# Kernel optimization log

Hardware: AMD Instinct MI355X
Metric: run time of the kernel (lower is better)

Reference implementation:

```python
import jax, jax.numpy as jnp
import numpy as np
from jax import lax

B, C, H, W = 32, 256, 96, 96
G = 2            # num_groups
K = 3            # kernel_size
R = 4            # reduction_ratio
CR = C // R
BN_EPS = 1e-5


def setup_inputs() -> dict:
    key = jax.random.key(0)
    ks = jax.random.split(key, 10)
    inp = {
        "x": jax.random.normal(ks[0], (B, C, H, W), dtype=jnp.float32),
        # dynamic depthwise weight bank and bias bank
        "dyn_weight": jax.random.normal(ks[1], (G, C, K, K), dtype=jnp.float32) * 0.02,
        "dyn_bias": jax.random.normal(ks[2], (G, C), dtype=jnp.float32) * 0.02,
        # proj: ConvModule(C -> C//R, 1x1, BN, GELU)  [conv has no bias since BN follows]
        "w1": jax.random.normal(ks[3], (CR, C), dtype=jnp.float32) * (1.0 / np.sqrt(C)),
        "bn_gamma": jnp.ones((CR,), dtype=jnp.float32),
        "bn_beta": jnp.zeros((CR,), dtype=jnp.float32),
        "bn_mean": jax.random.normal(ks[4], (CR,), dtype=jnp.float32) * 0.1,
        "bn_var": jax.random.uniform(ks[5], (CR,), dtype=jnp.float32, minval=0.5, maxval=1.5),
        # second 1x1 conv: C//R -> C*G, with bias
        "w2": jax.random.normal(ks[6], (C * G, CR), dtype=jnp.float32) * (1.0 / np.sqrt(CR)),
        "b2": jnp.zeros((C * G,), dtype=jnp.float32),
    }
    return inp


def _proj(p, w1, bn_gamma, bn_beta, bn_mean, bn_var, w2, b2):
    # p: [B, C, h, w] -> [B, C*G, h, w]; 1x1 conv -> BN(eval) -> GELU -> 1x1 conv
    h = jnp.einsum('bchw,oc->bohw', p, w1)
    inv = bn_gamma * lax.rsqrt(bn_var + BN_EPS)
    h = h * inv[None, :, None, None] + (bn_beta - bn_mean * inv)[None, :, None, None]
    h = jax.nn.gelu(h, approximate=False)
    return jnp.einsum('bohw,no->bnhw', h, w2) + b2[None, :, None, None]


def reference(x, dyn_weight, dyn_bias, w1, bn_gamma, bn_beta, bn_mean, bn_var, w2, b2):
    # AdaptiveAvgPool2d to (K, K); H, W divisible by K -> uniform block average
    pooled = x.reshape(B, C, K, H // K, K, W // K).mean(axis=(3, 5))  # [B,C,K,K]

    # per-sample depthwise weights via softmax mixture over G weight banks
    scale = _proj(pooled, w1, bn_gamma, bn_beta, bn_mean, bn_var, w2, b2)
    scale = jax.nn.softmax(scale.reshape(B, G, C, K, K), axis=1)
    weight = jnp.sum(scale * dyn_weight[None], axis=1)  # [B,C,K,K]

    # per-sample bias via global-average-pooled features
    gap = x.mean(axis=(2, 3), keepdims=True)  # [B,C,1,1]
    bscale = _proj(gap, w1, bn_gamma, bn_beta, bn_mean, bn_var, w2, b2)
    bscale = jax.nn.softmax(bscale.reshape(B, G, C), axis=1)
    bias = jnp.sum(bscale * dyn_bias[None], axis=1)  # [B,C]

    # grouped conv with groups = B*C (per-sample depthwise)
    xr = x.reshape(1, B * C, H, W)
    wr = weight.reshape(B * C, 1, K, K)
    y = lax.conv_general_dilated(
        xr, wr, window_strides=(1, 1),
        padding=[(K // 2, K // 2), (K // 2, K // 2)],
        feature_group_count=B * C,
        dimension_numbers=('NCHW', 'OIHW', 'NCHW'))
    return y.reshape(B, C, H, W) + bias[:, :, None, None]
```

## Files before the change

### kernel.cpp

```cpp
#include <hip/hip_runtime.h>
#include <math.h>

#define B_ 32
#define C_ 256
#define HW_ 96
#define G_ 2
#define K_ 3
#define CR_ 64
#define IMG_ (HW_*HW_)
#define BN_EPS 1e-5f

__global__ __launch_bounds__(256) void pool_kernel(const float* __restrict__ x,
                                                   float* __restrict__ pooled) {
    int wg = blockIdx.x;
    int bh = wg % 3;
    int bc = wg / 3;
    const float4* src = (const float4*)(x + (size_t)bc * IMG_ + (size_t)bh * 32 * HW_);
    int t = threadIdx.x;
    float a0 = 0.f, a1 = 0.f, a2 = 0.f;
    #pragma unroll
    for (int k = 0; k < 3; ++k) {
        int f = t + 256 * k;
        float4 v = src[f];
        float s = v.x + v.y + v.z + v.w;
        int colq = f % 24;
        int bin = colq >> 3;
        a0 += (bin == 0) ? s : 0.f;
        a1 += (bin == 1) ? s : 0.f;
        a2 += (bin == 2) ? s : 0.f;
    }
    #pragma unroll
    for (int off = 32; off > 0; off >>= 1) {
        a0 += __shfl_down(a0, off);
        a1 += __shfl_down(a1, off);
        a2 += __shfl_down(a2, off);
    }
    __shared__ float red[3][4];
    int wave = t >> 6, lane = t & 63;
    if (lane == 0) { red[0][wave] = a0; red[1][wave] = a1; red[2][wave] = a2; }
    __syncthreads();
    if (t < 3) {
        float s = red[t][0] + red[t][1] + red[t][2] + red[t][3];
        pooled[(size_t)bc * 9 + bh * 3 + t] = s * (1.0f / 1024.0f);
    }
}

__global__ __launch_bounds__(256) void proj_kernel(
    const float* __restrict__ pooled,
    const float* __restrict__ dyn_w,
    const float* __restrict__ dyn_b,
    const float* __restrict__ w1,
    const float* __restrict__ bn_g, const float* __restrict__ bn_b,
    const float* __restrict__ bn_m, const float* __restrict__ bn_v,
    const float* __restrict__ w2,
    const float* __restrict__ b2,
    float* __restrict__ wout,
    float* __restrict__ bout)
{
    int b = blockIdx.x;
    __shared__ float pool[C_][10];
    __shared__ float hbuf[CR_][10];
    int t = threadIdx.x;

    {
        const float* p = pooled + ((size_t)b * C_ + t) * 9;
        float s = 0.f;
        #pragma unroll
        for (int i = 0; i < 9; ++i) { float v = p[i]; pool[t][i] = v; s += v; }
        pool[t][9] = s * (1.0f / 9.0f);
    }
    __syncthreads();

    for (int task = t; task < CR_ * 10; task += 256) {
        int o = task & 63, pos = task >> 6;
        const float4* wr = (const float4*)(w1 + (size_t)o * C_);
        float acc = 0.f;
        #pragma unroll 8
        for (int i = 0; i < C_ / 4; ++i) {
            float4 wv = wr[i];
            acc += wv.x * pool[4*i][pos] + wv.y * pool[4*i+1][pos]
                 + wv.z * pool[4*i+2][pos] + wv.w * pool[4*i+3][pos];
        }
        float inv = bn_g[o] * rsqrtf(bn_v[o] + BN_EPS);
        float hv = acc * inv + (bn_b[o] - bn_m[o] * inv);
        hv = 0.5f * hv * (1.0f + erff(hv * 0.70710678118654752f));
        hbuf[o][pos] = hv;
    }
    __syncthreads();

    for (int task = t; task < C_ * 10; task += 256) {
        int c = task & 255, pos = task >> 8;
        const float4* r0 = (const float4*)(w2 + (size_t)c * CR_);
        const float4* r1 = (const float4*)(w2 + (size_t)(C_ + c) * CR_);
        float s0 = b2[c], s1 = b2[C_ + c];
        #pragma unroll 8
        for (int i = 0; i < CR_ / 4; ++i) {
            float4 v0 = r0[i], v1 = r1[i];
            float h0 = hbuf[4*i][pos], h1 = hbuf[4*i+1][pos];
            float h2 = hbuf[4*i+2][pos], h3 = hbuf[4*i+3][pos];
            s0 += v0.x*h0 + v0.y*h1 + v0.z*h2 + v0.w*h3;
            s1 += v1.x*h0 + v1.y*h1 + v1.z*h2 + v1.w*h3;
        }
        float m = fmaxf(s0, s1);
        float e0 = expf(s0 - m), e1 = expf(s1 - m);
        float p0 = e0 / (e0 + e1), p1 = 1.0f - p0;
        if (pos < 9) {
            wout[((size_t)b * C_ + c) * 9 + pos] =
                p0 * dyn_w[(size_t)c * 9 + pos] + p1 * dyn_w[(size_t)(C_ * 9) + c * 9 + pos];
        } else {
            bout[(size_t)b * C_ + c] = p0 * dyn_b[c] + p1 * dyn_b[C_ + c];
        }
    }
}

__global__ __launch_bounds__(192) void dwconv_kernel(const float* __restrict__ x,
                                                     const float* __restrict__ wgt,
                                                     const float* __restrict__ bias,
                                                     float* __restrict__ out) {
    int bc = blockIdx.x;
    int t = threadIdx.x;
    int qc = t % 24;
    int rg = t / 24;
    int r0 = rg * 12;

    const float* img = x + (size_t)bc * IMG_;
    float4* dst = (float4*)(out + (size_t)bc * IMG_);

    float w[9];
    #pragma unroll
    for (int i = 0; i < 9; ++i) w[i] = wgt[(size_t)bc * 9 + i];
    float bs = bias[bc];

    float A[6], Bv[6], Cv[6];

    #define LOADROW(r, d)                                                    \
        do {                                                                 \
            int _r = (r);                                                    \
            if ((unsigned)_r < (unsigned)HW_) {                              \
                const float* _p = img + _r * HW_ + 4 * qc;                   \
                float4 _v = *(const float4*)_p;                              \
                d[1] = _v.x; d[2] = _v.y; d[3] = _v.z; d[4] = _v.w;          \
                d[0] = (qc > 0)  ? _p[-1] : 0.f;                             \
                d[5] = (qc < 23) ? _p[4]  : 0.f;                             \
            } else {                                                         \
                d[0] = d[1] = d[2] = d[3] = d[4] = d[5] = 0.f;               \
            }                                                                \
        } while (0)

    LOADROW(r0 - 1, A);
    LOADROW(r0,     Bv);

    #pragma unroll
    for (int i = 0; i < 12; ++i) {
        int r = r0 + i;
        LOADROW(r + 1, Cv);
        float4 o;
        o.x = bs; o.y = bs; o.z = bs; o.w = bs;
        #pragma unroll
        for (int j = 0; j < 3; ++j) {
            o.x += A[j]  * w[j] + Bv[j]  * w[3+j] + Cv[j]  * w[6+j];
            o.y += A[j+1]* w[j] + Bv[j+1]* w[3+j] + Cv[j+1]* w[6+j];
            o.z += A[j+2]* w[j] + Bv[j+2]* w[3+j] + Cv[j+2]* w[6+j];
            o.w += A[j+3]* w[j] + Bv[j+3]* w[3+j] + Cv[j+3]* w[6+j];
        }
        dst[r * 24 + qc] = o;
        #pragma unroll
        for (int j = 0; j < 6; ++j) { A[j] = Bv[j]; Bv[j] = Cv[j]; }
    }
    #undef LOADROW
}

extern "C" void kernel_launch(void* const* d_in, const int* in_sizes, int n_in,
                              void* d_out, int out_size, void* d_ws, size_t ws_size,
                              hipStream_t stream) {
    const float* x     = (const float*)d_in[0];
    const float* dyn_w = (const float*)d_in[1];
    const float* dyn_b = (const float*)d_in[2];
    const float* w1    = (const float*)d_in[3];
    const float* bn_g  = (const float*)d_in[4];
    const float* bn_b  = (const float*)d_in[5];
    const float* bn_m  = (const float*)d_in[6];
    const float* bn_v  = (const float*)d_in[7];
    const float* w2    = (const float*)d_in[8];
    const float* b2    = (const float*)d_in[9];
    float* out = (float*)d_out;

    float* ws = (float*)d_ws;
    float* pooled = ws;
    float* weight = ws + (size_t)B_ * C_ * 9;
    float* bias   = weight + (size_t)B_ * C_ * 9;

    pool_kernel<<<B_ * C_ * 3, 256, 0, stream>>>(x, pooled);
    proj_kernel<<<B_, 256, 0, stream>>>(pooled, dyn_w, dyn_b, w1, bn_g, bn_b,
                                        bn_m, bn_v, w2, b2, weight, bias);
    dwconv_kernel<<<B_ * C_, 192, 0, stream>>>(x, weight, bias, out);
}
```

Baseline: 621.8 us.

## Parallelize projection over positions, reverse dwconv block order, use nontemporal stores

The projection kernel now launches one block per (position, batch) pair instead of one per batch, and splits the first 1x1 conv dot product across four lanes with a shuffle reduction. This raises parallelism in a kernel that previously ran only 32 blocks. The depthwise conv visits images in reverse order, so the last images pooled, likely still in cache, are read first. It also writes output with nontemporal stores so the streaming output does not evict input from cache.

```diff
diff --git a/kernel.cpp b/kernel.cpp
--- a/kernel.cpp
+++ b/kernel.cpp
@@ -9,6 +9,8 @@
 #define CR_ 64
 #define IMG_ (HW_*HW_)
 #define BN_EPS 1e-5f
+
+typedef float vfloat4 __attribute__((ext_vector_type(4)));
 
 __global__ __launch_bounds__(256) void pool_kernel(const float* __restrict__ x,
                                                    float* __restrict__ pooled) {
@@ -57,47 +59,64 @@
     float* __restrict__ wout,
     float* __restrict__ bout)
 {
-    int b = blockIdx.x;
-    __shared__ float pool[C_][10];
-    __shared__ float hbuf[CR_][10];
-    int t = threadIdx.x;
+    int pos = blockIdx.x;
+    int b   = blockIdx.y;
+    int t   = threadIdx.x;
+
+    __shared__ float spool[C_];
+    __shared__ float sh[CR_];
 
     {
         const float* p = pooled + ((size_t)b * C_ + t) * 9;
-        float s = 0.f;
-        #pragma unroll
-        for (int i = 0; i < 9; ++i) { float v = p[i]; pool[t][i] = v; s += v; }
-        pool[t][9] = s * (1.0f / 9.0f);
+        float v;
+        if (pos < 9) {
+            v = p[pos];
+        } else {
+            float s = 0.f;
+            #pragma unroll
+            for (int i = 0; i < 9; ++i) s += p[i];
+            v = s * (1.0f / 9.0f);
+        }
+        spool[t] = v;
     }
     __syncthreads();
 
-    for (int task = t; task < CR_ * 10; task += 256) {
-        int o = task & 63, pos = task >> 6;
-        const float4* wr = (const float4*)(w1 + (size_t)o * C_);
+    {
+        int o = t >> 2, sub = t & 3;
+        const float* wrow = w1 + (size_t)o * C_;
         float acc = 0.f;
-        #pragma unroll 8
-        for (int i = 0; i < C_ / 4; ++i) {
-            float4 wv = wr[i];
-            acc += wv.x * pool[4*i][pos] + wv.y * pool[4*i+1][pos]
-                 + wv.z * pool[4*i+2][pos] + wv.w * pool[4*i+3][pos];
-        }
-        float inv = bn_g[o] * rsqrtf(bn_v[o] + BN_EPS);
-        float hv = acc * inv + (bn_b[o] - bn_m[o] * inv);
-        hv = 0.5f * hv * (1.0f + erff(hv * 0.70710678118654752f));
-        hbuf[o][pos] = hv;
+        #pragma unroll
+        for (int cc = 0; cc < 4; ++cc) {
+            int base = cc * 64 + sub * 16;
+            const float4* wq = (const float4*)(wrow + base);
+            const float* pp = spool + base;
+            #pragma unroll
+            for (int i = 0; i < 4; ++i) {
+                float4 wv = wq[i];
+                acc += wv.x * pp[4*i]   + wv.y * pp[4*i+1]
+                     + wv.z * pp[4*i+2] + wv.w * pp[4*i+3];
+            }
+        }
+        acc += __shfl_xor(acc, 1);
+        acc += __shfl_xor(acc, 2);
+        if (sub == 0) {
+            float inv = bn_g[o] * rsqrtf(bn_v[o] + BN_EPS);
+            float hv = acc * inv + (bn_b[o] - bn_m[o] * inv);
+            hv = 0.5f * hv * (1.0f + erff(hv * 0.70710678118654752f));
+            sh[o] = hv;
+        }
     }
     __syncthreads();
 
-    for (int task = t; task < C_ * 10; task += 256) {
-        int c = task & 255, pos = task >> 8;
+    {
+        int c = t;
         const float4* r0 = (const float4*)(w2 + (size_t)c * CR_);
         const float4* r1 = (const float4*)(w2 + (size_t)(C_ + c) * CR_);
         float s0 = b2[c], s1 = b2[C_ + c];
-        #pragma unroll 8
+        #pragma unroll
         for (int i = 0; i < CR_ / 4; ++i) {
             float4 v0 = r0[i], v1 = r1[i];
-            float h0 = hbuf[4*i][pos], h1 = hbuf[4*i+1][pos];
-            float h2 = hbuf[4*i+2][pos], h3 = hbuf[4*i+3][pos];
+            float h0 = sh[4*i], h1 = sh[4*i+1], h2 = sh[4*i+2], h3 = sh[4*i+3];
             s0 += v0.x*h0 + v0.y*h1 + v0.z*h2 + v0.w*h3;
             s1 += v1.x*h0 + v1.y*h1 + v1.z*h2 + v1.w*h3;
         }
@@ -117,14 +136,14 @@
                                                      const float* __restrict__ wgt,
                                                      const float* __restrict__ bias,
                                                      float* __restrict__ out) {
-    int bc = blockIdx.x;
+    int bc = (B_ * C_ - 1) - blockIdx.x;
     int t = threadIdx.x;
     int qc = t % 24;
     int rg = t / 24;
     int r0 = rg * 12;
 
     const float* img = x + (size_t)bc * IMG_;
-    float4* dst = (float4*)(out + (size_t)bc * IMG_);
+    vfloat4* dst = (vfloat4*)(out + (size_t)bc * IMG_);
 
     float w[9];
     #pragma unroll
@@ -154,7 +173,7 @@
     for (int i = 0; i < 12; ++i) {
         int r = r0 + i;
         LOADROW(r + 1, Cv);
-        float4 o;
+        vfloat4 o;
         o.x = bs; o.y = bs; o.z = bs; o.w = bs;
         #pragma unroll
         for (int j = 0; j < 3; ++j) {
@@ -163,7 +182,7 @@
             o.z += A[j+2]* w[j] + Bv[j+2]* w[3+j] + Cv[j+2]* w[6+j];
             o.w += A[j+3]* w[j] + Bv[j+3]* w[3+j] + Cv[j+3]* w[6+j];
         }
-        dst[r * 24 + qc] = o;
+        __builtin_nontemporal_store(o, &dst[r * 24 + qc]);
         #pragma unroll
         for (int j = 0; j < 6; ++j) { A[j] = Bv[j]; Bv[j] = Cv[j]; }
     }
@@ -191,7 +210,7 @@
     float* bias   = weight + (size_t)B_ * C_ * 9;
 
     pool_kernel<<<B_ * C_ * 3, 256, 0, stream>>>(x, pooled);
-    proj_kernel<<<B_, 256, 0, stream>>>(pooled, dyn_w, dyn_b, w1, bn_g, bn_b,
-                                        bn_m, bn_v, w2, b2, weight, bias);
+    proj_kernel<<<dim3(10, B_), 256, 0, stream>>>(pooled, dyn_w, dyn_b, w1, bn_g, bn_b,
+                                                  bn_m, bn_v, w2, b2, weight, bias);
     dwconv_kernel<<<B_ * C_, 192, 0, stream>>>(x, weight, bias, out);
 }
```

Result: faster. 565.9 us (-9.0%).
